# Optimization experiments

Measured on AMD Instinct MI355X. Metric: run time of the kernel, lower is better.

Reference implementation:

```python
import jax, jax.numpy as jnp
import numpy as np

N = 20000      # num_nodes / scatter_size
F = 128        # dataset_num_features
H = 8          # heads
HID = 64       # hidden_channels
REP = 512      # represent_features
NCLS = 133     # dataset_num_classes
E = 200000     # num edges (== num synapses)
PTS = 4        # points per synapse
P = E * PTS    # total synapse points

# Eval-mode semantics: dropout = identity; PyG MLP BatchNorm with fresh
# running stats (mean=0, var=1, affine=1/0) = identity. GATConv has no
# edge_dim, so edge_attr does not enter the math (kept as an input for parity).

def _glorot(key, shape):
    fan_in, fan_out = shape[0], shape[-1]
    if len(shape) == 3:  # attention vectors [H, C]: PyG treats as (1, H*C)
        fan_in, fan_out = 1, shape[-2] * shape[-1]
    lim = jnp.sqrt(6.0 / (fan_in + fan_out))
    return jax.random.uniform(key, shape, jnp.float32, -lim, lim)


def setup_inputs() -> dict:
    key = jax.random.key(0)
    ks = jax.random.split(key, 20)
    edge_index = jax.random.randint(ks[0], (2, E), 0, N, dtype=jnp.int32)
    edge_attr = jax.random.normal(ks[1], (E, 1), jnp.float32)
    synapse = jax.random.normal(ks[2], (P, 6), jnp.float32)
    # every synapse (edge) owns PTS points -> no empty segments for max-pool
    synapse_index = (jnp.arange(P, dtype=jnp.int32) // PTS)
    inp = {
        "edge_index": edge_index,
        "edge_attr": edge_attr,
        "synapse": synapse,
        "synapse_index": synapse_index,
        "scatter_size": N,
        # learned node embedding (nn.Parameter, xavier)
        "x_param": _glorot(ks[3], (N, F)),
        # GATConv 1: F -> H*HID
        "W1": _glorot(ks[4], (F, H * HID)),
        "att_src1": _glorot(ks[5], (1, H, HID))[0],
        "att_dst1": _glorot(ks[6], (1, H, HID))[0],
        "b1": jnp.zeros((H * HID,), jnp.float32),
        # GATConv 2: H*HID -> REP, heads=1, concat=False
        "W2": _glorot(ks[7], (H * HID, REP)),
        "att_src2": _glorot(ks[8], (1, 1, REP))[0],
        "att_dst2": _glorot(ks[9], (1, 1, REP))[0],
        "b2": jnp.zeros((REP,), jnp.float32),
        # synapse_encoder MLP([6, 256, 512])
        "We1": _glorot(ks[10], (6, 256)),
        "be1": jnp.zeros((256,), jnp.float32),
        "We2": _glorot(ks[11], (256, 512)),
        "be2": jnp.zeros((512,), jnp.float32),
        # classmodel MLP([1536, 512, 133])
        "Wc1": _glorot(ks[12], (1536, 512)),
        "bc1": jnp.zeros((512,), jnp.float32),
        "Wc2": _glorot(ks[13], (512, NCLS)),
        "bc2": jnp.zeros((NCLS,), jnp.float32),
    }
    return inp


def _gat_conv(x, src, dst, n, W, a_src, a_dst, b, heads, ch, concat):
    # x: [n, Fin]; src/dst already include self-loops (PyG default)
    xl = (x @ W).reshape(n, heads, ch)                 # [n, H, C]
    s = jnp.einsum('nhc,hc->nh', xl, a_src)            # alpha_src
    d = jnp.einsum('nhc,hc->nh', xl, a_dst)            # alpha_dst
    alpha = jax.nn.leaky_relu(s[src] + d[dst], negative_slope=0.2)  # [Ee, H]
    amax = jax.ops.segment_max(alpha, dst, num_segments=n)
    ex = jnp.exp(alpha - amax[dst])
    den = jax.ops.segment_sum(ex, dst, num_segments=n)
    a = ex / (den[dst] + 1e-16)                        # segment softmax
    out = jax.ops.segment_sum(xl[src] * a[:, :, None], dst, num_segments=n)
    out = out.reshape(n, heads * ch) if concat else out.mean(axis=1)
    return out + b


def _scatter_mean(vals, idx, n):
    s = jax.ops.segment_sum(vals, idx, num_segments=n)
    cnt = jax.ops.segment_sum(jnp.ones((vals.shape[0],), vals.dtype), idx, num_segments=n)
    return s / jnp.maximum(cnt, 1.0)[:, None]


def reference(edge_index, edge_attr, synapse, synapse_index, scatter_size,
              x_param, W1, att_src1, att_dst1, b1, W2, att_src2, att_dst2, b2,
              We1, be1, We2, be2, Wc1, bc1, Wc2, bc2):
    n = scatter_size
    loop = jnp.arange(n, dtype=edge_index.dtype)
    src = jnp.concatenate([edge_index[0], loop])   # GATConv adds self-loops
    dst = jnp.concatenate([edge_index[1], loop])

    x = jax.nn.elu(_gat_conv(x_param, src, dst, n, W1, att_src1, att_dst1, b1, H, HID, True))
    x = _gat_conv(x, src, dst, n, W2, att_src2, att_dst2, b2, 1, REP, False)   # [n, REP]

    # global_max_pool over synapse points -> one 6-vec per edge
    x_point = jax.ops.segment_max(synapse, synapse_index, num_segments=E)      # [E, 6]
    x_point = jax.nn.relu(x_point @ We1 + be1) @ We2 + be2                      # [E, 512]

    left = _scatter_mean(x_point, edge_index[0], n)
    right = _scatter_mean(x_point, edge_index[1], n)

    final = jnp.concatenate([x, left, right], axis=1)                           # [n, 1536]
    pred = jax.nn.relu(final @ Wc1 + bc1) @ Wc2 + bc2
    return pred
```

## Files before the change

kernel.cpp:

```cpp
#include <hip/hip_runtime.h>
#include <cstddef>

#define NN   20000
#define FEAT 128
#define NH   8
#define NE   200000
#define EE   220000

typedef _Float16 f16;
typedef _Float16 f16x2 __attribute__((ext_vector_type(2)));
typedef _Float16 f16x4 __attribute__((ext_vector_type(4)));
typedef _Float16 f16x8 __attribute__((ext_vector_type(8)));
typedef float    f32x4 __attribute__((ext_vector_type(4)));

__device__ __forceinline__ float lrelu(float a) { return a > 0.f ? a : 0.2f * a; }
__device__ __forceinline__ float rdlane(float v, int l) {
  return __int_as_float(__builtin_amdgcn_readlane(__float_as_int(v), l));
}

#define QB0 128
#define QB1 (QB0 + 8)
#define QB2 (QB1 + 80)
#define QB3 (QB2 + 64)
#define QB4 (QB3 + 782)
#define QB5 (QB4 + 1250)
__global__ __launch_bounds__(256) void preamble(
    const int* __restrict__ ei, const float* __restrict__ syn,
    const float* __restrict__ W1, const float* __restrict__ xparam,
    const float* __restrict__ W2, const float* __restrict__ We2,
    const float* __restrict__ Wc1, const float* __restrict__ Wc2,
    const float* __restrict__ b2, const float* __restrict__ be2,
    const float* __restrict__ as2, const float* __restrict__ ad2,
    int* __restrict__ dL, int* __restrict__ dR,
    float* __restrict__ xp, f16* __restrict__ W1t, f16* __restrict__ xph,
    f16* __restrict__ WzAt, f16* __restrict__ McatT, f16* __restrict__ Wc2t,
    float* __restrict__ vB, float* __restrict__ vL, float* __restrict__ vR,
    float* __restrict__ ws2, float* __restrict__ wd2)
{
  __shared__ float smem[2112];
  const int b = blockIdx.x, t = threadIdx.x;
  if (b < QB0) {
    float (*As)[68] = (float(*)[68])smem;
    float (*Bs)[64] = (float(*)[64])(smem + 16 * 68);
    const int bb = b;
    const float* A; const float* B; f16* dst; int dstOff, m0, n0;
    if (bb < 64)      { A = W2;  B = Wc1;  dst = WzAt;  dstOff = 0;
                        m0 = (bb >> 3) * 64; n0 = (bb & 7) * 64; }
    else if (bb < 96) { int i = bb - 64; A = We2; B = Wc1 + (size_t)512 * 512;
                        dst = McatT; dstOff = 0;
                        m0 = (i >> 3) * 64; n0 = (i & 7) * 64; }
    else              { int i = bb - 96; A = We2; B = Wc1 + (size_t)1024 * 512;
                        dst = McatT; dstOff = 256;
                        m0 = (i >> 3) * 64; n0 = (i & 7) * 64; }
    const int tx = t & 15, ty = t >> 4;
    float acc[4][4] = {{0.f}};
    float pa[4], pb[4];
#pragma unroll
    for (int i = 0; i < 4; i++) {
      int idx = t + i * 256;
      pa[i] = A[(size_t)(m0 + (idx >> 4)) * 512 + (idx & 15)];
      pb[i] = B[(size_t)(idx >> 6) * 512 + n0 + (idx & 63)];
    }
    for (int k0 = 0; k0 < 512; k0 += 16) {
#pragma unroll
      for (int i = 0; i < 4; i++) {
        int idx = t + i * 256;
        As[idx & 15][idx >> 4] = pa[i];
        Bs[idx >> 6][idx & 63] = pb[i];
      }
      __syncthreads();
      if (k0 + 16 < 512) {
        int kn = k0 + 16;
#pragma unroll
        for (int i = 0; i < 4; i++) {
          int idx = t + i * 256;
          pa[i] = A[(size_t)(m0 + (idx >> 4)) * 512 + kn + (idx & 15)];
          pb[i] = B[(size_t)(kn + (idx >> 6)) * 512 + n0 + (idx & 63)];
        }
      }
#pragma unroll
      for (int kk = 0; kk < 16; kk++) {
        float4 a4 = *(const float4*)&As[kk][ty * 4];
        float4 b4 = *(const float4*)&Bs[kk][tx * 4];
        float av[4] = {a4.x, a4.y, a4.z, a4.w};
        float bv[4] = {b4.x, b4.y, b4.z, b4.w};
#pragma unroll
        for (int i = 0; i < 4; i++)
#pragma unroll
          for (int j = 0; j < 4; j++) acc[i][j] = fmaf(av[i], bv[j], acc[i][j]);
      }
      __syncthreads();
    }
#pragma unroll
    for (int i = 0; i < 4; i++)
#pragma unroll
      for (int j = 0; j < 4; j++)
        dst[(size_t)(n0 + tx * 4 + j) * 512 + dstOff + m0 + ty * 4 + i] = (f16)acc[i][j];
  } else if (b < QB1) {
    int g = (b - QB0) * 256 + t;
    int seg = g >> 9, j = g & 511;
    if (seg == 0) {
      float a = 0.f;
      for (int k = 0; k < 512; k++) a = fmaf(b2[k], Wc1[(size_t)k * 512 + j], a);
      vB[j] = a;
    } else if (seg == 1) {
      float a = 0.f;
      for (int k = 0; k < 512; k++) a = fmaf(be2[k], Wc1[(size_t)(512 + k) * 512 + j], a);
      vL[j] = a;
    } else if (seg == 2) {
      float a = 0.f;
      for (int k = 0; k < 512; k++) a = fmaf(be2[k], Wc1[(size_t)(1024 + k) * 512 + j], a);
      vR[j] = a;
    } else {
      float a = 0.f, c2 = 0.f;
      for (int c = 0; c < 512; c++) {
        float w = W2[(size_t)j * 512 + c];
        a = fmaf(w, as2[c], a);
        c2 = fmaf(w, ad2[c], c2);
      }
      ws2[j] = a; wd2[j] = c2;
    }
  } else if (b < QB2) {
    float (*tile)[33] = (float(*)[33])smem;
    int i0 = b - QB1;
    const int n0 = (i0 % 5) * 32, k0 = (i0 / 5) * 32;
    const int tx = t & 31, ty = t >> 5;
#pragma unroll
    for (int i = 0; i < 4; i++) {
      int k = k0 + ty + i * 8, n = n0 + tx;
      tile[ty + i * 8][tx] = (n < 133) ? Wc2[(size_t)k * 133 + n] : 0.f;
    }
    __syncthreads();
#pragma unroll
    for (int i = 0; i < 4; i++) {
      int n = n0 + ty + i * 8, k = k0 + tx;
      if (n < 133) Wc2t[(size_t)n * 512 + k] = (f16)tile[tx][ty + i * 8];
    }
  } else if (b < QB3) {
    float (*tile)[33] = (float(*)[33])smem;
    int bb = b - QB2;
    const int n0 = (bb & 15) * 32, k0 = (bb >> 4) * 32;
    const int tx = t & 31, ty = t >> 5;
#pragma unroll
    for (int i = 0; i < 4; i++)
      tile[ty + i * 8][tx] = W1[(size_t)(k0 + ty + i * 8) * 512 + n0 + tx];
    __syncthreads();
#pragma unroll
    for (int i = 0; i < 4; i++)
      W1t[(size_t)(n0 + ty + i * 8) * 128 + k0 + tx] = (f16)tile[tx][ty + i * 8];
  } else if (b < QB4) {
    int e = (b - QB3) * 256 + t;
    if (e >= NE) return;
    const float* p = syn + (size_t)e * 24;
    float v[24];
#pragma unroll
    for (int i = 0; i < 6; i++) {
      float4 q = *(const float4*)(p + i * 4);
      v[i*4+0] = q.x; v[i*4+1] = q.y; v[i*4+2] = q.z; v[i*4+3] = q.w;
    }
#pragma unroll
    for (int dd = 0; dd < 6; dd++)
      xp[(size_t)e * 6 + dd] = fmaxf(fmaxf(v[dd], v[6 + dd]), fmaxf(v[12 + dd], v[18 + dd]));
    atomicAdd(&dL[ei[e]], 1);
    atomicAdd(&dR[ei[NE + e]], 1);
  } else {
    int idx = ((b - QB4) * 256 + t) * 8;
    float4 q0 = *(const float4*)(xparam + idx);
    float4 q1 = *(const float4*)(xparam + idx + 4);
    f16x8 o;
    o[0] = (f16)q0.x; o[1] = (f16)q0.y; o[2] = (f16)q0.z; o[3] = (f16)q0.w;
    o[4] = (f16)q1.x; o[5] = (f16)q1.y; o[6] = (f16)q1.z; o[7] = (f16)q1.w;
    *(f16x8*)(xph + idx) = o;
  }
}

__global__ __launch_bounds__(256) void fused1(
    const f16* __restrict__ xph, const f16* __restrict__ W1t, f16* __restrict__ xl1h,
    const float* __restrict__ xp, const float* __restrict__ We1,
    const float* __restrict__ be1,
    const int* __restrict__ oL, const int* __restrict__ eL,
    const int* __restrict__ oR, const int* __restrict__ eR,
    f16* __restrict__ hlrh)
{
  __shared__ __align__(16) f16 smem[7680];
  const int t = threadIdx.x;
  if (blockIdx.x < 1252) {
    f16 (*As)[40] = (f16(*)[40])smem;
    f16 (*Bs)[40] = (f16(*)[40])(smem + 64 * 40);
    const int wave = t >> 6, lane = t & 63;
    const int quad = lane >> 4, mrow = lane & 15;
    const int m0 = (blockIdx.x >> 2) * 64, n0 = (blockIdx.x & 3) * 128;
    f32x4 acc[4][2];
    f32x4 zero4 = {0.f, 0.f, 0.f, 0.f};
#pragma unroll
    for (int i = 0; i < 4; i++)
#pragma unroll
      for (int j = 0; j < 2; j++) acc[i][j] = zero4;
    const int ar = t >> 2, ac = (t & 3) * 8;
    for (int k0 = 0; k0 < FEAT; k0 += 32) {
      {
        int gm = m0 + ar;
        f16x8 v = {0, 0, 0, 0, 0, 0, 0, 0};
        if (gm < NN) v = *(const f16x8*)(xph + (size_t)gm * FEAT + k0 + ac);
        *(f16x8*)&As[ar][ac] = v;
      }
#pragma unroll
      for (int i = 0; i < 2; i++) {
        int idx = t + i * 256;
        int r = idx >> 2, c = (idx & 3) * 8;
        *(f16x8*)&Bs[r][c] = *(const f16x8*)(W1t + (size_t)(n0 + r) * FEAT + k0 + c);
      }
      __syncthreads();
      f16x8 af[4], bf[2];
#pragma unroll
      for (int mt = 0; mt < 4; mt++) af[mt] = *(const f16x8*)&As[mt * 16 + mrow][quad * 8];
#pragma unroll
      for (int nt = 0; nt < 2; nt++) bf[nt] = *(const f16x8*)&Bs[wave * 32 + nt * 16 + mrow][quad * 8];
#pragma unroll
      for (int mt = 0; mt < 4; mt++)
#pragma unroll
        for (int nt = 0; nt < 2; nt++)
          acc[mt][nt] = __builtin_amdgcn_mfma_f32_16x16x32_f16(af[mt], bf[nt], acc[mt][nt], 0, 0, 0);
      __syncthreads();
    }
#pragma unroll
    for (int mt = 0; mt < 4; mt++)
#pragma unroll
      for (int nt = 0; nt < 2; nt++) {
        int col = n0 + wave * 32 + nt * 16 + mrow;
#pragma unroll
        for (int reg = 0; reg < 4; reg++) {
          int row = m0 + mt * 16 + quad * 4 + reg;
          if (row < NN) xl1h[(size_t)row * 512 + col] = (f16)acc[mt][nt][reg];
        }
      }
  } else {
    const int wave = t >> 6, lane = t & 63;
    const int w = (blockIdx.x - 1252) * 4 + wave;
    float4 wv[6];
#pragma unroll
    for (int j = 0; j < 6; j++) wv[j] = *(const float4*)(We1 + j * 256 + 4 * lane);
    const float4 bv = *(const float4*)(be1 + 4 * lane);
#pragma unroll 1
    for (int i = 0; i < 4; i++) {
      const int b = w + i * 10000;
      const int* off; const int* lst; int n;
      if (b < NN) { off = oL; lst = eL; n = b; } else { off = oR; lst = eR; n = b - NN; }
      const int beg = off[n], deg = off[n + 1] - beg;
      float a0 = 0.f, a1 = 0.f, a2 = 0.f, a3 = 0.f;
      for (int base = 0; base < deg; base += 32) {
        const int m = min(32, deg - base);
        float x0 = 0.f, x1 = 0.f, x2 = 0.f, x3 = 0.f, x4 = 0.f, x5 = 0.f;
        if (lane < m) {
          const int e = lst[beg + base + lane];
          const float* pr = xp + (size_t)e * 6;
          float2 p0 = *(const float2*)pr;
          float2 p1 = *(const float2*)(pr + 2);
          float2 p2 = *(const float2*)(pr + 4);
          x0 = p0.x; x1 = p0.y; x2 = p1.x; x3 = p1.y; x4 = p2.x; x5 = p2.y;
        }
        const int ms = __builtin_amdgcn_readfirstlane(m);
        for (int s = 0; s < ms; s++) {
          const float f0 = rdlane(x0, s), f1 = rdlane(x1, s), f2 = rdlane(x2, s);
          const float f3 = rdlane(x3, s), f4 = rdlane(x4, s), f5 = rdlane(x5, s);
          float v0 = bv.x, v1 = bv.y, v2 = bv.z, v3 = bv.w;
          v0 = fmaf(f0, wv[0].x, v0); v1 = fmaf(f0, wv[0].y, v1);
          v2 = fmaf(f0, wv[0].z, v2); v3 = fmaf(f0, wv[0].w, v3);
          v0 = fmaf(f1, wv[1].x, v0); v1 = fmaf(f1, wv[1].y, v1);
          v2 = fmaf(f1, wv[1].z, v2); v3 = fmaf(f1, wv[1].w, v3);
          v0 = fmaf(f2, wv[2].x, v0); v1 = fmaf(f2, wv[2].y, v1);
          v2 = fmaf(f2, wv[2].z, v2); v3 = fmaf(f2, wv[2].w, v3);
          v0 = fmaf(f3, wv[3].x, v0); v1 = fmaf(f3, wv[3].y, v1);
          v2 = fmaf(f3, wv[3].z, v2); v3 = fmaf(f3, wv[3].w, v3);
          v0 = fmaf(f4, wv[4].x, v0); v1 = fmaf(f4, wv[4].y, v1);
          v2 = fmaf(f4, wv[4].z, v2); v3 = fmaf(f4, wv[4].w, v3);
          v0 = fmaf(f5, wv[5].x, v0); v1 = fmaf(f5, wv[5].y, v1);
          v2 = fmaf(f5, wv[5].z, v2); v3 = fmaf(f5, wv[5].w, v3);
          a0 += fmaxf(v0, 0.f); a1 += fmaxf(v1, 0.f);
          a2 += fmaxf(v2, 0.f); a3 += fmaxf(v3, 0.f);
        }
      }
      const float rn = deg > 0 ? 1.f / (float)deg : 0.f;
      f16x4 o;
      o[0] = (f16)(a0 * rn); o[1] = (f16)(a1 * rn);
      o[2] = (f16)(a2 * rn); o[3] = (f16)(a3 * rn);
      *(f16x4*)(hlrh + (size_t)b * 256 + 4 * lane) = o;
    }
  }
}

__global__ __launch_bounds__(256) void fused2(
    const f16* __restrict__ x1h, const f16* __restrict__ WzAt, f16* __restrict__ zh,
    const f16* __restrict__ hlrh, const f16* __restrict__ McatT,
    const int* __restrict__ degL, const int* __restrict__ degR,
    const float* __restrict__ bc1, const float* __restrict__ vB,
    const float* __restrict__ vL, const float* __restrict__ vR, f16* __restrict__ Ph)
{
  __shared__ __align__(16) f16 smem[20480];
  const int t = threadIdx.x;
  const int logical = (blockIdx.x & 7) * 157 + (blockIdx.x >> 3);
  const bool isZ = logical < 628;
  const int bb = isZ ? logical : logical - 628;
  const int wave = t >> 6, lane = t & 63;
  const int wr = wave >> 1, wc = wave & 1;
  const int quad = lane >> 4, mrow = lane & 15;
  const int m0 = (bb >> 2) * 128, n0 = (bb & 3) * 128;
  f32x4 acc[4][4];
  f32x4 zero4 = {0.f, 0.f, 0.f, 0.f};
#pragma unroll
  for (int i = 0; i < 4; i++)
#pragma unroll
    for (int j = 0; j < 4; j++) acc[i][j] = zero4;
  const f16* Bt = isZ ? WzAt : McatT;
  const int r0 = t >> 2, r1 = (t + 256) >> 2;
  const int cc = (t & 3) * 8;
  const int gm0 = m0 + r0, gm1 = m0 + r1;

  auto loadA = [&](int k0, int gm) -> f16x8 {
    f16x8 v = {0, 0, 0, 0, 0, 0, 0, 0};
    if (gm < NN) {
      if (isZ) v = *(const f16x8*)(x1h + (size_t)gm * 512 + k0 + cc);
      else {
        size_t row = (k0 >> 8) ? (size_t)(NN + gm) : (size_t)gm;
        v = *(const f16x8*)(hlrh + row * 256 + (k0 & 255) + cc);
      }
    }
    return v;
  };
  auto loadB = [&](int k0, int r) -> f16x8 {
    return *(const f16x8*)(Bt + (size_t)(n0 + r) * 512 + k0 + cc);
  };

  f16x8 ra0 = loadA(0, gm0), ra1 = loadA(0, gm1);
  f16x8 rb0 = loadB(0, r0),  rb1 = loadB(0, r1);
#pragma unroll 1
  for (int it = 0; it < 16; ++it) {
    f16 (*As)[40] = (f16(*)[40])(smem + (it & 1) * 10240);
    f16 (*Bs)[40] = (f16(*)[40])(smem + (it & 1) * 10240 + 5120);
    *(f16x8*)&As[r0][cc] = ra0;
    *(f16x8*)&As[r1][cc] = ra1;
    *(f16x8*)&Bs[r0][cc] = rb0;
    *(f16x8*)&Bs[r1][cc] = rb1;
    __syncthreads();
    if (it < 15) {
      int kn = (it + 1) * 32;
      ra0 = loadA(kn, gm0); ra1 = loadA(kn, gm1);
      rb0 = loadB(kn, r0);  rb1 = loadB(kn, r1);
    }
    f16x8 af[4], bf[4];
#pragma unroll
    for (int mt = 0; mt < 4; mt++) af[mt] = *(const f16x8*)&As[wr * 64 + mt * 16 + mrow][quad * 8];
#pragma unroll
    for (int nt = 0; nt < 4; nt++) bf[nt] = *(const f16x8*)&Bs[wc * 64 + nt * 16 + mrow][quad * 8];
#pragma unroll
    for (int mt = 0; mt < 4; mt++)
#pragma unroll
      for (int nt = 0; nt < 4; nt++)
        acc[mt][nt] = __builtin_amdgcn_mfma_f32_16x16x32_f16(af[mt], bf[nt], acc[mt][nt], 0, 0, 0);
  }
  if (isZ) {
#pragma unroll
    for (int mt = 0; mt < 4; mt++)
#pragma unroll
      for (int nt = 0; nt < 4; nt++) {
        int col = n0 + wc * 64 + nt * 16 + mrow;
#pragma unroll
        for (int reg = 0; reg < 4; reg++) {
          int row = m0 + wr * 64 + mt * 16 + quad * 4 + reg;
          if (row < NN) zh[(size_t)row * 512 + col] = (f16)acc[mt][nt][reg];
        }
      }
  } else {
#pragma unroll
    for (int mt = 0; mt < 4; mt++)
#pragma unroll
      for (int nt = 0; nt < 4; nt++) {
        int col = n0 + wc * 64 + nt * 16 + mrow;
        float bb2 = bc1[col] + vB[col];
        float vl = vL[col], vr = vR[col];
#pragma unroll
        for (int reg = 0; reg < 4; reg++) {
          int row = m0 + wr * 64 + mt * 16 + quad * 4 + reg;
          if (row >= NN) continue;
          float v = acc[mt][nt][reg] + bb2;
          if (degL[row] > 0) v += vl;
          if (degR[row] > 0) v += vr;
          Ph[(size_t)row * 512 + col] = (f16)v;
        }
      }
  }
}

__global__ __launch_bounds__(256) void mfma_out(
    const f16* __restrict__ A, const f16* __restrict__ Bt,
    const float* __restrict__ bias, float* __restrict__ C, int M)
{
  __shared__ __align__(16) f16 As[64][40];
  __shared__ __align__(16) f16 Bs[128][40];
  const int t = threadIdx.x;
  const int wave = t >> 6, lane = t & 63;
  const int quad = lane >> 4, mrow = lane & 15;
  const int m0 = blockIdx.y * 64, n0 = blockIdx.x * 128;
  f32x4 acc[4][2];
  f32x4 zero4 = {0.f, 0.f, 0.f, 0.f};
#pragma unroll
  for (int i = 0; i < 4; i++)
#pragma unroll
    for (int j = 0; j < 2; j++) acc[i][j] = zero4;
  const int ar = t >> 2, ac = (t & 3) * 8;
  for (int k0 = 0; k0 < 512; k0 += 32) {
    {
      int gm = m0 + ar;
      f16x8 v = {0, 0, 0, 0, 0, 0, 0, 0};
      if (gm < M) v = *(const f16x8*)(A + (size_t)gm * 512 + k0 + ac);
      *(f16x8*)&As[ar][ac] = v;
    }
#pragma unroll
    for (int i = 0; i < 2; i++) {
      int idx = t + i * 256;
      int r = idx >> 2, c = (idx & 3) * 8;
      f16x8 v = {0, 0, 0, 0, 0, 0, 0, 0};
      if (n0 + r < 133) v = *(const f16x8*)(Bt + (size_t)(n0 + r) * 512 + k0 + c);
      *(f16x8*)&Bs[r][c] = v;
    }
    __syncthreads();
    f16x8 af[4], bf[2];
#pragma unroll
    for (int mt = 0; mt < 4; mt++) af[mt] = *(const f16x8*)&As[mt * 16 + mrow][quad * 8];
#pragma unroll
    for (int nt = 0; nt < 2; nt++) bf[nt] = *(const f16x8*)&Bs[wave * 32 + nt * 16 + mrow][quad * 8];
#pragma unroll
    for (int mt = 0; mt < 4; mt++)
#pragma unroll
      for (int nt = 0; nt < 2; nt++)
        acc[mt][nt] = __builtin_amdgcn_mfma_f32_16x16x32_f16(af[mt], bf[nt], acc[mt][nt], 0, 0, 0);
    __syncthreads();
  }
#pragma unroll
  for (int mt = 0; mt < 4; mt++)
#pragma unroll
    for (int nt = 0; nt < 2; nt++) {
      int col = n0 + wave * 32 + nt * 16 + mrow;
      if (col >= 133) continue;
      float bb = bias[col];
#pragma unroll
      for (int reg = 0; reg < 4; reg++) {
        int row = m0 + mt * 16 + quad * 4 + reg;
        if (row < M) C[(size_t)row * 133 + col] = acc[mt][nt][reg] + bb;
      }
    }
}

__global__ __launch_bounds__(1024) void scan_csr(
    const int* __restrict__ dL, const int* __restrict__ dR,
    int* __restrict__ oL, int* __restrict__ oR, int* __restrict__ oA)
{
  const int b = blockIdx.x;
  const int* deg = b == 0 ? dL : dR;
  __shared__ int part[1024];
  const int t = threadIdx.x;
  const int chunk = 20;
  int base = t * chunk;
  int sum = 0;
  for (int i = 0; i < chunk; i++) { int idx = base + i; if (idx < NN) sum += deg[idx]; }
  part[t] = sum;
  __syncthreads();
  for (int o = 1; o < 1024; o <<= 1) {
    int v = (t >= o) ? part[t - o] : 0;
    __syncthreads();
    part[t] += v;
    __syncthreads();
  }
  int run = part[t] - sum;
  if (b == 0) {
    for (int i = 0; i < chunk; i++) {
      int idx = base + i;
      if (idx < NN) { oL[idx] = run; run += deg[idx]; }
    }
    if (t == 0) oL[NN] = part[1023];
  } else {
    for (int i = 0; i < chunk; i++) {
      int idx = base + i;
      if (idx < NN) { oR[idx] = run; oA[idx] = run + idx; run += deg[idx]; }
    }
    if (t == 0) { oR[NN] = part[1023]; oA[NN] = part[1023] + NN; }
  }
}

__global__ __launch_bounds__(256) void fill_csr(
    const int* __restrict__ ei,
    const int* __restrict__ oL, const int* __restrict__ oR, const int* __restrict__ oA,
    int* __restrict__ cL, int* __restrict__ cR,
    int* __restrict__ eL, int* __restrict__ eR, int* __restrict__ snA)
{
  int e = blockIdx.x * 256 + threadIdx.x;
  if (e >= EE) return;
  if (e < NE) {
    int s = ei[e], d = ei[NE + e];
    int p = atomicAdd(&cL[s], 1); eL[oL[s] + p] = e;
    p = atomicAdd(&cR[d], 1);
    eR[oR[d] + p] = e;
    snA[oA[d] + 1 + p] = s;
  } else {
    int n = e - NE;
    snA[oA[n]] = n;
  }
}

__global__ __launch_bounds__(256) void attn_dots1(
    const f16* __restrict__ xlh, const float* __restrict__ asrc,
    const float* __restrict__ adst, float* __restrict__ s, float* __restrict__ d)
{
  int gid = blockIdx.x * 256 + threadIdx.x;
  if (gid >= NN * NH) return;
  int n = gid >> 3, h = gid & 7;
  const f16x2* row = (const f16x2*)(xlh + (size_t)n * 512 + h * 64);
  const float* a1 = asrc + h * 64;
  const float* a2 = adst + h * 64;
  float ss = 0.f, dd = 0.f;
#pragma unroll 8
  for (int j = 0; j < 32; j++) {
    f16x2 p = row[j];
    float v0 = (float)p[0], v1 = (float)p[1];
    ss += v0 * a1[2 * j] + v1 * a1[2 * j + 1];
    dd += v0 * a2[2 * j] + v1 * a2[2 * j + 1];
  }
  s[gid] = ss; d[gid] = dd;
}

__global__ __launch_bounds__(256) void gat_gather1(
    const int* __restrict__ snA, const int* __restrict__ offA,
    const float* __restrict__ s1, const float* __restrict__ d1,
    const f16* __restrict__ xlh, const float* __restrict__ b1,
    const float* __restrict__ ws2, const float* __restrict__ wd2,
    f16* __restrict__ x1h, float* __restrict__ s2, float* __restrict__ d2)
{
  __shared__ int sns[32];
  __shared__ float wls[256];
  __shared__ float red[256], redD[256];
  const int n = blockIdx.x, t = threadIdx.x;
  const int hw = t & 7;
  const int slot = t >> 3;
  const int hf = t >> 5;
  const int beg = offA[n], end = offA[n + 1];
  const int deg = end - beg;
  const float dnw = d1[n * 8 + hw];
  float a0 = 0.f, a1v = 0.f, denp = 0.f;
  for (int base = 0; base < deg; base += 32) {
    int m = min(32, deg - base);
    if (t < 32) sns[t] = (t < m) ? snA[beg + base + t] : 0;
    __syncthreads();
    {
      float w = 0.f;
      if (slot < m) w = __expf(lrelu(s1[sns[slot] * 8 + hw] + dnw));
      wls[t] = w;
      denp += w;
    }
    __syncthreads();
    int m8 = (m + 7) & ~7;
    for (int k = 0; k < m8; k += 8) {
      int ss[8]; float ww[8]; f16x2 pp[8];
#pragma unroll
      for (int u = 0; u < 8; u++) { ss[u] = sns[k + u]; ww[u] = wls[(k + u) * 8 + hf]; }
#pragma unroll
      for (int u = 0; u < 8; u++) pp[u] = *(const f16x2*)(xlh + (size_t)ss[u] * 512 + 2 * t);
#pragma unroll
      for (int u = 0; u < 8; u++) {
        a0  = fmaf(ww[u], (float)pp[u][0], a0);
        a1v = fmaf(ww[u], (float)pp[u][1], a1v);
      }
    }
    __syncthreads();
  }
  red[t] = denp;
  __syncthreads();
  for (int off = 128; off >= 8; off >>= 1) {
    if (t < off) red[t] += red[t + off];
    __syncthreads();
  }
  float rh = 1.f / (red[hf] + 1e-16f);
  __syncthreads();
  float v0 = a0 * rh + b1[2 * t], v1 = a1v * rh + b1[2 * t + 1];
  v0 = v0 > 0.f ? v0 : (__expf(v0) - 1.f);
  v1 = v1 > 0.f ? v1 : (__expf(v1) - 1.f);
  f16x2 o; o[0] = (f16)v0; o[1] = (f16)v1;
  *(f16x2*)(x1h + (size_t)n * 512 + 2 * t) = o;
  red[t]  = v0 * ws2[2 * t] + v1 * ws2[2 * t + 1];
  redD[t] = v0 * wd2[2 * t] + v1 * wd2[2 * t + 1];
  __syncthreads();
  for (int off = 128; off > 0; off >>= 1) {
    if (t < off) { red[t] += red[t + off]; redD[t] += redD[t + off]; }
    __syncthreads();
  }
  if (t == 0) { s2[n] = red[0]; d2[n] = redD[0]; }
}

__global__ __launch_bounds__(256) void gat_gather2(
    const int* __restrict__ snA, const int* __restrict__ offA,
    const float* __restrict__ s2, const float* __restrict__ d2,
    const f16* __restrict__ zh, const f16* __restrict__ Ph,
    f16* __restrict__ h2h)
{
  __shared__ int sns[32];
  __shared__ float wls[32];
  __shared__ float den_sh;
  const int n = blockIdx.x, t = threadIdx.x;
  const int beg = offA[n], end = offA[n + 1];
  const int deg = end - beg;
  const float dn = d2[n];
  float a0 = 0.f, a1v = 0.f, denp = 0.f;
  for (int base = 0; base < deg; base += 32) {
    int m = min(32, deg - base);
    if (t < 32) {
      int sn = (t < m) ? snA[beg + base + t] : 0;
      float w = (t < m) ? __expf(lrelu(s2[sn] + dn)) : 0.f;
      sns[t] = sn;
      wls[t] = w;
      denp += w;
    }
    __syncthreads();
    int m8 = (m + 7) & ~7;
    for (int k = 0; k < m8; k += 8) {
      int ss[8]; float ww[8]; f16x2 pp[8];
#pragma unroll
      for (int u = 0; u < 8; u++) { ss[u] = sns[k + u]; ww[u] = wls[k + u]; }
#pragma unroll
      for (int u = 0; u < 8; u++) pp[u] = *(const f16x2*)(zh + (size_t)ss[u] * 512 + 2 * t);
#pragma unroll
      for (int u = 0; u < 8; u++) {
        a0  = fmaf(ww[u], (float)pp[u][0], a0);
        a1v = fmaf(ww[u], (float)pp[u][1], a1v);
      }
    }
    __syncthreads();
  }
  if (t < 64) {
    denp += __shfl_xor(denp, 16);
    denp += __shfl_xor(denp, 8);
    denp += __shfl_xor(denp, 4);
    denp += __shfl_xor(denp, 2);
    denp += __shfl_xor(denp, 1);
    if (t == 0) den_sh = denp;
  }
  __syncthreads();
  float rn = 1.f / (den_sh + 1e-16f);
  f16x2 pv = *(const f16x2*)(Ph + (size_t)n * 512 + 2 * t);
  float v0 = fmaxf(a0  * rn + (float)pv[0], 0.f);
  float v1 = fmaxf(a1v * rn + (float)pv[1], 0.f);
  f16x2 o; o[0] = (f16)v0; o[1] = (f16)v1;
  *(f16x2*)(h2h + (size_t)n * 512 + 2 * t) = o;
}

extern "C" void kernel_launch(void* const* d_in, const int* in_sizes, int n_in,
                              void* d_out, int out_size, void* d_ws, size_t ws_size,
                              hipStream_t stream) {
  const int*   edge_index = (const int*)d_in[0];
  const float* synapse    = (const float*)d_in[2];
  const float* x_param = (const float*)d_in[5];
  const float* W1      = (const float*)d_in[6];
  const float* as1     = (const float*)d_in[7];
  const float* ad1     = (const float*)d_in[8];
  const float* b1      = (const float*)d_in[9];
  const float* W2      = (const float*)d_in[10];
  const float* as2     = (const float*)d_in[11];
  const float* ad2     = (const float*)d_in[12];
  const float* b2      = (const float*)d_in[13];
  const float* We1     = (const float*)d_in[14];
  const float* be1     = (const float*)d_in[15];
  const float* We2     = (const float*)d_in[16];
  const float* be2     = (const float*)d_in[17];
  const float* Wc1     = (const float*)d_in[18];
  const float* bc1     = (const float*)d_in[19];
  const float* Wc2     = (const float*)d_in[20];
  const float* bc2     = (const float*)d_in[21];
  float* out_p = (float*)d_out;

  char* p = (char*)d_ws;
  float* xp    = (float*)p; p += (size_t)NE * 6 * 4;
  float* s1    = (float*)p; p += (size_t)NN * 8 * 4;
  float* d1    = (float*)p; p += (size_t)NN * 8 * 4;
  float* s2    = (float*)p; p += (size_t)NN * 4;
  float* d2    = (float*)p; p += (size_t)NN * 4;
  float* vB    = (float*)p; p += 512 * 4;
  float* vL    = (float*)p; p += 512 * 4;
  float* vR    = (float*)p; p += 512 * 4;
  float* ws2   = (float*)p; p += 512 * 4;
  float* wd2   = (float*)p; p += 512 * 4;
  f16* xph     = (f16*)p; p += (size_t)NN * FEAT * 2;
  f16* xl1h    = (f16*)p; p += (size_t)NN * 512 * 2;
  f16* x1h     = (f16*)p; p += (size_t)NN * 512 * 2;
  f16* zh      = (f16*)p; p += (size_t)NN * 512 * 2;
  f16* h2h     = (f16*)p; p += (size_t)NN * 512 * 2;
  f16* Phb     = (f16*)p; p += (size_t)NN * 512 * 2;
  f16* hlrh    = (f16*)p; p += (size_t)2 * NN * 256 * 2;
  f16* W1t     = (f16*)p; p += (size_t)512 * FEAT * 2;
  f16* WzAt    = (f16*)p; p += (size_t)512 * 512 * 2;
  f16* McatT   = (f16*)p; p += (size_t)512 * 512 * 2;
  f16* Wc2t    = (f16*)p; p += (size_t)133 * 512 * 2;
  int* degL    = (int*)p;
  int* degR    = degL + NN;
  int* curL    = degR + NN;
  int* curR    = curL + NN;
  int* offL    = curR + NN;
  int* offR    = offL + NN + 1;
  int* offA    = offR + NN + 1;
  int* edgeL   = offA + NN + 1;
  int* edgeR   = edgeL + NE;
  int* snA     = edgeR + NE;

  hipMemsetAsync(degL, 0, (size_t)4 * NN * sizeof(int), stream);

  preamble<<<QB5, 256, 0, stream>>>(
      edge_index, synapse, W1, x_param, W2, We2, Wc1, Wc2, b2, be2, as2, ad2,
      degL, degR, xp, W1t, xph, WzAt, McatT, Wc2t, vB, vL, vR, ws2, wd2);
  scan_csr<<<2, 1024, 0, stream>>>(degL, degR, offL, offR, offA);
  fill_csr<<<(EE + 255) / 256, 256, 0, stream>>>(edge_index, offL, offR, offA,
                                                 curL, curR, edgeL, edgeR, snA);
  fused1<<<1252 + 2500, 256, 0, stream>>>(xph, W1t, xl1h, xp, We1, be1,
                                          offL, edgeL, offR, edgeR, hlrh);
  attn_dots1<<<(NN * NH + 255) / 256, 256, 0, stream>>>(xl1h, as1, ad1, s1, d1);
  gat_gather1<<<NN, 256, 0, stream>>>(snA, offA, s1, d1, xl1h, b1, ws2, wd2,
                                      x1h, s2, d2);
  fused2<<<1256, 256, 0, stream>>>(x1h, WzAt, zh, hlrh, McatT,
                                   degL, degR, bc1, vB, vL, vR, Phb);
  gat_gather2<<<NN, 256, 0, stream>>>(snA, offA, s2, d2, zh, Phb, h2h);
  mfma_out<<<dim3(2, 313), 256, 0, stream>>>(h2h, Wc2t, bc2, out_p, NN);
}
```

Baseline: 447.6 us.

## Replace LDS-staged block GEMM in fused2 with per-wave direct-load tiles

The fused2 GEMM no longer stages A and B tiles through double-buffered shared memory with block-wide barriers. Each wave now owns an independent 64x64 output tile and loads its MFMA operands straight from global memory into registers. The grid shrinks to exactly cover the wave-tile count. This removes LDS traffic and __syncthreads, but operands are no longer shared across the four waves of a block, so more global/L2 traffic is issued. Row loads past NN are not guarded, so padded tiles read beyond the valid rows.

```diff
diff --git a/kernel.cpp b/kernel.cpp
--- a/kernel.cpp
+++ b/kernel.cpp
@@ -296,77 +296,58 @@
     const float* __restrict__ bc1, const float* __restrict__ vB,
     const float* __restrict__ vL, const float* __restrict__ vR, f16* __restrict__ Ph)
 {
-  __shared__ __align__(16) f16 smem[20480];
   const int t = threadIdx.x;
-  const int logical = (blockIdx.x & 7) * 157 + (blockIdx.x >> 3);
-  const bool isZ = logical < 628;
-  const int bb = isZ ? logical : logical - 628;
   const int wave = t >> 6, lane = t & 63;
-  const int wr = wave >> 1, wc = wave & 1;
   const int quad = lane >> 4, mrow = lane & 15;
-  const int m0 = (bb >> 2) * 128, n0 = (bb & 3) * 128;
+  const int xcd = blockIdx.x & 7, bi = blockIdx.x >> 3;
+  const int logical = (xcd < 4 ? xcd * 157 : 4 * 157 + (xcd - 4) * 156) + bi;
+  const int gw = logical * 4 + wave;
+  const bool isZ = gw < 2504;
+  const int wt = isZ ? gw : gw - 2504;
+  const int R0 = (wt >> 3) * 64, C0 = (wt & 7) * 64;
+  const f16* Bt = isZ ? WzAt : McatT;
   f32x4 acc[4][4];
   f32x4 zero4 = {0.f, 0.f, 0.f, 0.f};
 #pragma unroll
   for (int i = 0; i < 4; i++)
 #pragma unroll
     for (int j = 0; j < 4; j++) acc[i][j] = zero4;
-  const f16* Bt = isZ ? WzAt : McatT;
-  const int r0 = t >> 2, r1 = (t + 256) >> 2;
-  const int cc = (t & 3) * 8;
-  const int gm0 = m0 + r0, gm1 = m0 + r1;
-
-  auto loadA = [&](int k0, int gm) -> f16x8 {
-    f16x8 v = {0, 0, 0, 0, 0, 0, 0, 0};
-    if (gm < NN) {
-      if (isZ) v = *(const f16x8*)(x1h + (size_t)gm * 512 + k0 + cc);
-      else {
-        size_t row = (k0 >> 8) ? (size_t)(NN + gm) : (size_t)gm;
-        v = *(const f16x8*)(hlrh + row * 256 + (k0 & 255) + cc);
-      }
-    }
-    return v;
-  };
-  auto loadB = [&](int k0, int r) -> f16x8 {
-    return *(const f16x8*)(Bt + (size_t)(n0 + r) * 512 + k0 + cc);
-  };
-
-  f16x8 ra0 = loadA(0, gm0), ra1 = loadA(0, gm1);
-  f16x8 rb0 = loadB(0, r0),  rb1 = loadB(0, r1);
+
 #pragma unroll 1
-  for (int it = 0; it < 16; ++it) {
-    f16 (*As)[40] = (f16(*)[40])(smem + (it & 1) * 10240);
-    f16 (*Bs)[40] = (f16(*)[40])(smem + (it & 1) * 10240 + 5120);
-    *(f16x8*)&As[r0][cc] = ra0;
-    *(f16x8*)&As[r1][cc] = ra1;
-    *(f16x8*)&Bs[r0][cc] = rb0;
-    *(f16x8*)&Bs[r1][cc] = rb1;
-    __syncthreads();
-    if (it < 15) {
-      int kn = (it + 1) * 32;
-      ra0 = loadA(kn, gm0); ra1 = loadA(kn, gm1);
-      rb0 = loadB(kn, r0);  rb1 = loadB(kn, r1);
-    }
-    f16x8 af[4], bf[4];
-#pragma unroll
-    for (int mt = 0; mt < 4; mt++) af[mt] = *(const f16x8*)&As[wr * 64 + mt * 16 + mrow][quad * 8];
-#pragma unroll
-    for (int nt = 0; nt < 4; nt++) bf[nt] = *(const f16x8*)&Bs[wc * 64 + nt * 16 + mrow][quad * 8];
+  for (int ph = 0; ph < 2; ++ph) {
+    const f16* pa[4]; const f16* pb[4];
+#pragma unroll
+    for (int mt = 0; mt < 4; mt++) {
+      int rowA = R0 + mt * 16 + mrow;
+      pa[mt] = isZ ? x1h + (size_t)rowA * 512 + ph * 256 + quad * 8
+                   : hlrh + (size_t)(ph ? NN + rowA : rowA) * 256 + quad * 8;
+    }
+#pragma unroll
+    for (int nt = 0; nt < 4; nt++)
+      pb[nt] = Bt + (size_t)(C0 + nt * 16 + mrow) * 512 + ph * 256 + quad * 8;
+#pragma unroll 2
+    for (int ks = 0; ks < 8; ++ks) {
+      f16x8 af[4], bf[4];
+#pragma unroll
+      for (int mt = 0; mt < 4; mt++) af[mt] = *(const f16x8*)(pa[mt] + ks * 32);
+#pragma unroll
+      for (int nt = 0; nt < 4; nt++) bf[nt] = *(const f16x8*)(pb[nt] + ks * 32);
+#pragma unroll
+      for (int mt = 0; mt < 4; mt++)
+#pragma unroll
+        for (int nt = 0; nt < 4; nt++)
+          acc[mt][nt] = __builtin_amdgcn_mfma_f32_16x16x32_f16(af[mt], bf[nt], acc[mt][nt], 0, 0, 0);
+    }
+  }
+  if (isZ) {
 #pragma unroll
     for (int mt = 0; mt < 4; mt++)
 #pragma unroll
-      for (int nt = 0; nt < 4; nt++)
-        acc[mt][nt] = __builtin_amdgcn_mfma_f32_16x16x32_f16(af[mt], bf[nt], acc[mt][nt], 0, 0, 0);
-  }
-  if (isZ) {
-#pragma unroll
-    for (int mt = 0; mt < 4; mt++)
-#pragma unroll
       for (int nt = 0; nt < 4; nt++) {
-        int col = n0 + wc * 64 + nt * 16 + mrow;
+        int col = C0 + nt * 16 + mrow;
 #pragma unroll
         for (int reg = 0; reg < 4; reg++) {
-          int row = m0 + wr * 64 + mt * 16 + quad * 4 + reg;
+          int row = R0 + mt * 16 + quad * 4 + reg;
           if (row < NN) zh[(size_t)row * 512 + col] = (f16)acc[mt][nt][reg];
         }
       }
@@ -375,12 +356,12 @@
     for (int mt = 0; mt < 4; mt++)
 #pragma unroll
       for (int nt = 0; nt < 4; nt++) {
-        int col = n0 + wc * 64 + nt * 16 + mrow;
+        int col = C0 + nt * 16 + mrow;
         float bb2 = bc1[col] + vB[col];
         float vl = vL[col], vr = vR[col];
 #pragma unroll
         for (int reg = 0; reg < 4; reg++) {
-          int row = m0 + wr * 64 + mt * 16 + quad * 4 + reg;
+          int row = R0 + mt * 16 + quad * 4 + reg;
           if (row >= NN) continue;
           float v = acc[mt][nt][reg] + bb2;
           if (degL[row] > 0) v += vl;
@@ -721,7 +702,7 @@
   attn_dots1<<<(NN * NH + 255) / 256, 256, 0, stream>>>(xl1h, as1, ad1, s1, d1);
   gat_gather1<<<NN, 256, 0, stream>>>(snA, offA, s1, d1, xl1h, b1, ws2, wd2,
                                       x1h, s2, d2);
-  fused2<<<1256, 256, 0, stream>>>(x1h, WzAt, zh, hlrh, McatT,
+  fused2<<<1252, 256, 0, stream>>>(x1h, WzAt, zh, hlrh, McatT,
                                    degL, degR, bc1, vB, vL, vR, Phb);
   gat_gather2<<<NN, 256, 0, stream>>>(snA, offA, s2, d2, zh, Phb, h2h);
   mfma_out<<<dim3(2, 313), 256, 0, stream>>>(h2h, Wc2t, bc2, out_p, NN);
```

Result: slower. 481.5 us (+7.6%).
